# Optimization experiments

Hardware: AMD Instinct MI355X
Metric: run time of the kernel (lower is better)

The kernel has to match this reference:

```python
import jax, jax.numpy as jnp
import numpy as np

B, L, E, H, V, DT, C = 64, 80, 256, 256, 30000, 100, 4
D = 4 * L * H  # BatchNorm / FC feature dim = max_length * hidden * 4
EPS = 1e-5


def setup_inputs() -> dict:
    key = jax.random.key(0)
    ks = jax.random.split(key, 20)
    n = lambda k, shape, s: jax.random.normal(k, shape, jnp.float32) * s
    g = 1.0 / np.sqrt(H)  # pytorch LSTM init scale
    return {
        "arg1": jax.random.randint(ks[0], (B, L), 0, V, dtype=jnp.int32),
        "arg2": jax.random.randint(ks[1], (B, L), 0, V, dtype=jnp.int32),
        "seq_lengths": jnp.full((B,), L, dtype=jnp.int32),
        "transE1": jax.random.normal(ks[2], (L, DT), jnp.float32),
        "transE2": jax.random.normal(ks[3], (L, DT), jnp.float32),
        # learned parameters
        "table": n(ks[4], (V, E), 0.05),                 # embedding (xavier-ish)
        "Wih_f": n(ks[5], (4 * H, E), g),
        "Whh_f": n(ks[6], (4 * H, H), g),
        "bih_f": n(ks[7], (4 * H,), g),
        "bhh_f": n(ks[8], (4 * H,), g),
        "Wih_b": n(ks[9], (4 * H, E), g),
        "Whh_b": n(ks[10], (4 * H, H), g),
        "bih_b": n(ks[11], (4 * H,), g),
        "bhh_b": n(ks[12], (4 * H,), g),
        "R": jax.random.uniform(ks[13], (2 * E, 2 * E), jnp.float32),  # torch.rand init
        "gamma": jnp.ones((D,), jnp.float32),
        "beta": jnp.zeros((D,), jnp.float32),
        "fcW": n(ks[14], (C, D), 0.01),
        "fcb": jnp.zeros((C,), jnp.float32),
    }


def _lstm_dir(x, Wih, Whh, b):
    # x: (B, L, E); pytorch gate order i, f, g, o
    xg = jnp.einsum('ble,ge->blg', x, Wih) + b          # (B, L, 4H)
    xg = jnp.swapaxes(xg, 0, 1)                         # (L, B, 4H)
    h0 = jnp.zeros((x.shape[0], Whh.shape[1]), x.dtype)

    def step(carry, g_t):
        h, c = carry
        gates = g_t + h @ Whh.T
        i, f, gg, o = jnp.split(gates, 4, axis=-1)
        c = jax.nn.sigmoid(f) * c + jax.nn.sigmoid(i) * jnp.tanh(gg)
        h = jax.nn.sigmoid(o) * jnp.tanh(c)
        return (h, c), h

    _, hs = jax.lax.scan(step, (h0, h0), xg)
    return jnp.swapaxes(hs, 0, 1)                       # (B, L, H)


def _bilstm(x, Wih_f, Whh_f, bih_f, bhh_f, Wih_b, Whh_b, bih_b, bhh_b):
    fwd = _lstm_dir(x, Wih_f, Whh_f, bih_f + bhh_f)
    bwd = _lstm_dir(x[:, ::-1], Wih_b, Whh_b, bih_b + bhh_b)[:, ::-1]
    return jnp.concatenate([fwd, bwd], axis=-1)         # (B, L, 2H)


def _forward(arg1, arg2, transE1, transE2, table, Wih_f, Whh_f, bih_f, bhh_f,
             Wih_b, Whh_b, bih_b, bhh_b, R, gamma, beta, fcW, fcb):
    # deal_transE: relation[i,j] = tanh(mean(arg1_word_i - arg2_word_j));
    # identical for every batch element -> block-diagonal kron.
    m1 = transE1.mean(axis=1)                           # (L,)
    m2 = transE2.mean(axis=1)                           # (L,)
    rel = jnp.tanh(m1[:, None] - m2[None, :])           # (L, L)
    kg = jax.lax.stop_gradient(jnp.kron(jnp.eye(B, dtype=rel.dtype), rel))  # (B*L, B*L)

    e1 = table[arg1]                                    # (B, L, E); dropout p=0 -> identity
    e2 = table[arg2]
    o1 = _bilstm(e1, Wih_f, Whh_f, bih_f, bhh_f, Wih_b, Whh_b, bih_b, bhh_b)
    o2 = _bilstm(e2, Wih_f, Whh_f, bih_f, bhh_f, Wih_b, Whh_b, bih_b, bhh_b)

    N = B * L
    t1 = o1.reshape(N, 2 * H)
    t2 = o2.reshape(N, 2 * H)

    last = jnp.tanh((t1 @ R) @ t2.T) + kg               # (N, N)
    sf1 = jax.nn.softmax(last, axis=1).mean(axis=0)[:, None]  # (N, 1)
    sf2 = jax.nn.softmax(last, axis=0).mean(axis=1)[:, None]  # (N, 1)

    out1 = (t1 * sf2).reshape(B, L, 2 * H)
    out2 = (t2 * sf1).reshape(B, L, 2 * H)
    out = jnp.concatenate([out1, out2], axis=1).reshape(B, -1)  # (B, D)

    # BatchNorm1d in training mode (biased variance over batch)
    mu = out.mean(axis=0)
    var = out.var(axis=0)
    xn = (out - mu) / jnp.sqrt(var + EPS) * gamma + beta

    logits = xn @ fcW.T + fcb
    return jax.nn.log_softmax(logits, axis=1)           # (B, C)


def reference(arg1, arg2, seq_lengths, transE1, transE2, table, Wih_f, Whh_f,
              bih_f, bhh_f, Wih_b, Whh_b, bih_b, bhh_b, R, gamma, beta, fcW, fcb):
    del seq_lengths  # only encodes (B, L), which are static here
    return _forward(arg1, arg2, transE1, transE2, table, Wih_f, Whh_f, bih_f,
                    bhh_f, Wih_b, Whh_b, bih_b, bhh_b, R, gamma, beta, fcW, fcb)
```

## Files before the change

### kernel.cpp

```cpp
#include <hip/hip_runtime.h>
#include <cstddef>
#include <cstdint>

typedef unsigned short ushort_t;

constexpr int B_ = 64, L_ = 80, E_ = 256, H_ = 256, C_ = 4, DT_ = 100;
constexpr int N_ = B_ * L_;
constexpr int G4_ = 4 * H_;
constexpr int DH2_ = 2 * H_;
constexpr int DF_ = 4 * L_ * H_;
constexpr float EPS_ = 1e-5f;
constexpr int FB_USH = 8192;

typedef short s8v __attribute__((ext_vector_type(8)));
typedef float f4v __attribute__((ext_vector_type(4)));
typedef ushort_t us8 __attribute__((ext_vector_type(8)));

__device__ inline ushort_t f2bf_rn(float x) {
    uint32_t u = __builtin_bit_cast(uint32_t, x);
    uint32_t r = (u + 0x7fffu + ((u >> 16) & 1u)) >> 16;
    return (ushort_t)r;
}
__device__ inline float bf2f(ushort_t h) {
    uint32_t u = ((uint32_t)h) << 16;
    return __builtin_bit_cast(float, u);
}
__device__ inline float bf2f_lo(uint32_t u) { return __builtin_bit_cast(float, u << 16); }
__device__ inline float bf2f_hi(uint32_t u) { return __builtin_bit_cast(float, u & 0xffff0000u); }
__device__ inline float rcpf(float x) { return __builtin_amdgcn_rcpf(x); }
__device__ inline float sigm(float x) { return rcpf(1.f + __expf(-x)); }
__device__ inline float tanh_fast(float x) {
    float e2 = __expf(2.f * x);
    return 1.f - 2.f * rcpf(1.f + e2);
}

#define MFMA_B16(a, b, c) __builtin_amdgcn_mfma_f32_16x16x32_bf16((a), (b), (c), 0, 0, 0)

__global__ void k_prep(const int* __restrict__ arg1, const int* __restrict__ arg2,
                       const float* __restrict__ table,
                       const float* __restrict__ tE1, const float* __restrict__ tE2,
                       const float* __restrict__ Wih_f, const float* __restrict__ Wih_b,
                       const float* __restrict__ bih_f, const float* __restrict__ bhh_f,
                       const float* __restrict__ bih_b, const float* __restrict__ bhh_b,
                       const float* __restrict__ R,
                       const float* __restrict__ Whh_f, const float* __restrict__ Whh_b,
                       ushort_t* __restrict__ ehi, ushort_t* __restrict__ elo,
                       ushort_t* __restrict__ Wchi, ushort_t* __restrict__ Wclo,
                       float* __restrict__ bcat,
                       ushort_t* __restrict__ Rthi, ushort_t* __restrict__ Rtlo,
                       ushort_t* __restrict__ Bhi, ushort_t* __restrict__ Blo,
                       ushort_t* __restrict__ fragbuf, int* __restrict__ flags,
                       float* __restrict__ rel) {
    __shared__ float m1[80], m2[80];
    int blk = blockIdx.x;
    int tid = threadIdx.x;
    if (blk < 10240) {
        int r = blk;
        int rr = (r >= N_) ? (r - N_) : r;
        int idx = (r >= N_) ? arg2[rr] : arg1[rr];
        float v = table[(size_t)idx * E_ + tid];
        ushort_t h = f2bf_rn(v);
        ehi[(size_t)r * E_ + tid] = h;
        elo[(size_t)r * E_ + tid] = f2bf_rn(v - bf2f(h));
    } else if (blk < 12288) {
        int i = (blk - 10240) * 256 + tid;
        if (i < 2 * G4_ * E_) {
            float v = (i < G4_ * E_) ? Wih_f[i] : Wih_b[i - G4_ * E_];
            ushort_t h = f2bf_rn(v);
            Wchi[i] = h;
            Wclo[i] = f2bf_rn(v - bf2f(h));
        }
        if (i < 2 * G4_)
            bcat[i] = (i < G4_) ? (bih_f[i] + bhh_f[i]) : (bih_b[i - G4_] + bhh_b[i - G4_]);
        if (i < 512 * 512) {
            int m = i >> 9, k = i & 511;
            float v = R[k * 512 + m];
            ushort_t h = f2bf_rn(v);
            Rthi[i] = h;
            Rtlo[i] = f2bf_rn(v - bf2f(h));
        }
    } else if (blk < 14336) {
        int idx = (blk - 12288) * 256 + tid;
        int e = idx & 7;
        int lane = (idx >> 3) & 63;
        int g = (idx >> 9) & 3;
        int kt = (idx >> 11) & 7;
        int w = (idx >> 14) & 15;
        int d = idx >> 18;
        int c = lane & 15, q = lane >> 4;
        int row = g * 256 + w * 16 + c;
        int k = kt * 32 + q * 8 + e;
        const float* W = d ? Whh_b : Whh_f;
        float v = W[row * 256 + k];
        ushort_t hi = f2bf_rn(v);
        Bhi[idx] = hi;
        Blo[idx] = f2bf_rn(v - bf2f(hi));
    } else if (blk < 14400) {
        int i = (blk - 14336) * 256 + tid;
        if (i < 1024) flags[i] = 0;
        uint4* p = (uint4*)fragbuf;
        for (int jj = i; jj < 32768; jj += 64 * 256)
            p[jj] = make_uint4(0u, 0u, 0u, 0u);
    } else {
        if (tid < 80) {
            float s = 0.f;
            for (int k = 0; k < DT_; ++k) s += tE1[tid * DT_ + k];
            m1[tid] = s * (1.0f / DT_);
        } else if (tid < 160) {
            int i = tid - 80;
            float s = 0.f;
            for (int k = 0; k < DT_; ++k) s += tE2[i * DT_ + k];
            m2[i] = s * (1.0f / DT_);
        }
        __syncthreads();
        for (int idx = tid; idx < 80 * 80; idx += 256)
            rel[idx] = tanhf(m1[idx / 80] - m2[idx % 80]);
    }
}

__global__ __launch_bounds__(256, 2) void k_lstm9c(
        const float* __restrict__ xg,
        const ushort_t* __restrict__ Bhi, const ushort_t* __restrict__ Blo,
        ushort_t* __restrict__ o1hi, ushort_t* __restrict__ o1lo,
        ushort_t* __restrict__ o2hi, ushort_t* __restrict__ o2lo,
        ushort_t* __restrict__ fragbuf, int* __restrict__ flags) {
    const int bid = blockIdx.x;
    const int s = bid & 15;
    const int cg = (bid >> 4) & 7;
    const int d = bid >> 7;
    const int tid = threadIdx.x;
    const int g = tid >> 6, lane = tid & 63;
    const int c16 = lane & 15, qq = lane >> 4;

    __shared__ __align__(16) ushort_t Abuf[8192];
    __shared__ float pre[4][16][16];

    s8v bh[8], bl[8];
    {
        const s8v* BH = (const s8v*)Bhi;
        const s8v* BL = (const s8v*)Blo;
        int base = (d * 16 + s) * 2048 + g * 64 + lane;
        #pragma unroll
        for (int kt = 0; kt < 8; ++kt) {
            bh[kt] = BH[base + kt * 256];
            bl[kt] = BL[base + kt * 256];
        }
    }

    const int c_loc = tid >> 4, j = tid & 15;
    const int kglob = s * 16 + j;
    const int p_kt = kglob >> 5;
    const int p_q = (kglob & 31) >> 3, p_e = kglob & 7;
    const int p_lane = c_loc | (p_q << 4);
    const int fb_off = (p_kt * 64 + p_lane) * 8 + p_e;
    const int cc = cg * 16 + c_loc;
    const int w = cc >> 6, bb = cc & 63;
    ushort_t* ophi = w ? o2hi : o1hi;
    ushort_t* oplo = w ? o2lo : o1lo;
    float cst = 0.f;

    const int grp = bid >> 4;
    int* gflags = flags + grp * 16;
    const size_t fbbase = (size_t)grp * 2 * FB_USH;

    for (int t = 0; t < L_; ++t) {
        int l = d ? (L_ - 1 - t) : t;

        float xv[4];
        {
            const float* xp = xg + (size_t)(w * N_ + bb * L_ + l) * 2048
                              + d * 1024 + kglob;
            #pragma unroll
            for (int gg = 0; gg < 4; ++gg) xv[gg] = xp[gg * 256];
        }

        if (t > 0) {
            if (tid < 16) {
                while (__hip_atomic_load(&gflags[tid], __ATOMIC_RELAXED,
                                         __HIP_MEMORY_SCOPE_AGENT) < t)
                    __builtin_amdgcn_s_sleep(2);
            }
            __syncthreads();
        }

        {
            const unsigned long long* src = (const unsigned long long*)(fragbuf
                + fbbase + (size_t)(t & 1) * FB_USH);
            unsigned long long* dst = (unsigned long long*)Abuf;
            #pragma unroll
            for (int r = 0; r < 8; ++r)
                dst[r * 256 + tid] = __hip_atomic_load(
                    &src[r * 256 + tid], __ATOMIC_RELAXED,
                    __HIP_MEMORY_SCOPE_AGENT);
        }
        __syncthreads();

        f4v acc = {0.f, 0.f, 0.f, 0.f};
        {
            const s8v* AH = (const s8v*)&Abuf[0];
            const s8v* AL = (const s8v*)&Abuf[4096];
            #pragma unroll
            for (int kt = 0; kt < 8; ++kt) {
                s8v ah = AH[kt * 64 + lane];
                s8v al = AL[kt * 64 + lane];
                acc = MFMA_B16(ah, bh[kt], acc);
                acc = MFMA_B16(ah, bl[kt], acc);
                acc = MFMA_B16(al, bh[kt], acc);
            }
        }
        #pragma unroll
        for (int r = 0; r < 4; ++r)
            pre[g][qq * 4 + r][c16] = acc[r];
        __syncthreads();

        ushort_t hh, hl;
        size_t oidx;
        {
            float pi = pre[0][c_loc][j] + xv[0];
            float pf = pre[1][c_loc][j] + xv[1];
            float pg = pre[2][c_loc][j] + xv[2];
            float po = pre[3][c_loc][j] + xv[3];
            float si = sigm(pi), sf_ = sigm(pf), so = sigm(po);
            cst = sf_ * cst + si * tanh_fast(pg);
            float h = so * tanh_fast(cst);
            oidx = (size_t)(bb * L_ + l) * DH2_ + d * H_ + kglob;
            hh = f2bf_rn(h);
            hl = f2bf_rn(h - bf2f(hh));
            ushort_t* fbn = fragbuf + fbbase + (size_t)((t + 1) & 1) * FB_USH;
            __hip_atomic_store(&fbn[fb_off], hh, __ATOMIC_RELAXED,
                               __HIP_MEMORY_SCOPE_AGENT);
            __hip_atomic_store(&fbn[4096 + fb_off], hl, __ATOMIC_RELAXED,
                               __HIP_MEMORY_SCOPE_AGENT);
        }
        __syncthreads();

        if (tid == 0)
            __hip_atomic_store(&flags[bid], t + 1, __ATOMIC_RELAXED,
                               __HIP_MEMORY_SCOPE_AGENT);

        ophi[oidx] = hh;
        oplo[oidx] = hl;
    }
}

__global__ __launch_bounds__(256) void k_gemm_bf(
        const ushort_t* __restrict__ Ahi, const ushort_t* __restrict__ Alo,
        const ushort_t* __restrict__ Bthi, const ushort_t* __restrict__ Btlo,
        const float* __restrict__ bias, float* __restrict__ Cout,
        ushort_t* __restrict__ Couthi, ushort_t* __restrict__ Coutlo,
        int M, int Nn, int K) {
    __shared__ ushort_t smpool[4][4096];
    const int tid = threadIdx.x;
    const int w = tid >> 6, lane = tid & 63;
    const int wr = w >> 1, wc = w & 1;
    const int c16 = lane & 15, q4 = lane >> 4;
    const int nbx = Nn >> 7;
    const int cpx = ((M >> 7) * nbx) >> 3;
    const int fid = blockIdx.x;
    const int swz = (fid & 7) * cpx + (fid >> 3);
    const int bx = swz % nbx, by = swz / nbx;
    const int r0 = by * 128, c0 = bx * 128;

    f4v acc[4][4] = {};
    const ushort_t* planes[4] = {
        Ahi + (size_t)r0 * K, Alo + (size_t)r0 * K,
        Bthi + (size_t)c0 * K, Btlo + (size_t)c0 * K };

    for (int kk = 0; kk < K; kk += 32) {
        #pragma unroll
        for (int p = 0; p < 4; ++p) {
            const ushort_t* src = planes[p] + kk;
            #pragma unroll
            for (int it = 0; it < 2; ++it) {
                int idx = it * 256 + tid;
                int row = idx >> 2, q = idx & 3;
                *(us8*)&smpool[p][(q * 128 + row) * 8] =
                    *(const us8*)&src[(size_t)row * K + q * 8];
            }
        }
        __syncthreads();
        s8v ah[4], al[4], bhv[4], blv[4];
        #pragma unroll
        for (int mi = 0; mi < 4; ++mi) {
            int ar = wr * 64 + mi * 16 + c16;
            ah[mi] = *(const s8v*)&smpool[0][(q4 * 128 + ar) * 8];
            al[mi] = *(const s8v*)&smpool[1][(q4 * 128 + ar) * 8];
        }
        #pragma unroll
        for (int ni = 0; ni < 4; ++ni) {
            int br = wc * 64 + ni * 16 + c16;
            bhv[ni] = *(const s8v*)&smpool[2][(q4 * 128 + br) * 8];
            blv[ni] = *(const s8v*)&smpool[3][(q4 * 128 + br) * 8];
        }
        #pragma unroll
        for (int mi = 0; mi < 4; ++mi)
            #pragma unroll
            for (int ni = 0; ni < 4; ++ni) {
                acc[mi][ni] = MFMA_B16(ah[mi], bhv[ni], acc[mi][ni]);
                acc[mi][ni] = MFMA_B16(ah[mi], blv[ni], acc[mi][ni]);
                acc[mi][ni] = MFMA_B16(al[mi], bhv[ni], acc[mi][ni]);
            }
        __syncthreads();
    }
    #pragma unroll
    for (int mi = 0; mi < 4; ++mi)
        #pragma unroll
        for (int rg = 0; rg < 4; ++rg) {
            int row = r0 + wr * 64 + mi * 16 + q4 * 4 + rg;
            #pragma unroll
            for (int ni = 0; ni < 4; ++ni) {
                int col = c0 + wc * 64 + ni * 16 + c16;
                float v = acc[mi][ni][rg] + (bias ? bias[col] : 0.f);
                size_t idx = (size_t)row * Nn + col;
                if (Couthi) {
                    ushort_t h = f2bf_rn(v);
                    Couthi[idx] = h;
                    Coutlo[idx] = f2bf_rn(v - bf2f(h));
                } else {
                    Cout[idx] = v;
                }
            }
        }
}

__global__ __launch_bounds__(256) void k_bigm(
        const ushort_t* __restrict__ uhi, const ushort_t* __restrict__ ulo,
        const ushort_t* __restrict__ vhi, const ushort_t* __restrict__ vlo,
        const float* __restrict__ rel, ushort_t* __restrict__ Ebf,
        float* __restrict__ rowpart, float* __restrict__ colpart) {
    __shared__ ushort_t smpool[4][4096];
    const int tid = threadIdx.x;
    const int w = tid >> 6, lane = tid & 63;
    const int wr = w >> 1, wc = w & 1;
    const int c16 = lane & 15, q4 = lane >> 4;
    const int fid = blockIdx.x;
    const int swz = (fid & 7) * 200 + (fid >> 3);
    const int bx = swz % 40, by = swz / 40;
    const int r0 = by * 128, c0 = bx * 128;

    f4v acc[4][4] = {};
    const ushort_t* planes[4] = {
        uhi + (size_t)r0 * DH2_, ulo + (size_t)r0 * DH2_,
        vhi + (size_t)c0 * DH2_, vlo + (size_t)c0 * DH2_ };

    for (int kk = 0; kk < 16; ++kk) {
        #pragma unroll
        for (int p = 0; p < 4; ++p) {
            const ushort_t* src = planes[p] + kk * 32;
            #pragma unroll
            for (int it = 0; it < 2; ++it) {
                int idx = it * 256 + tid;
                int row = idx >> 2, q = idx & 3;
                *(us8*)&smpool[p][(q * 128 + row) * 8] =
                    *(const us8*)&src[(size_t)row * DH2_ + q * 8];
            }
        }
        __syncthreads();
        s8v ah[4], al[4], bhv[4], blv[4];
        #pragma unroll
        for (int mi = 0; mi < 4; ++mi) {
            int ar = wr * 64 + mi * 16 + c16;
            ah[mi] = *(const s8v*)&smpool[0][(q4 * 128 + ar) * 8];
            al[mi] = *(const s8v*)&smpool[1][(q4 * 128 + ar) * 8];
        }
        #pragma unroll
        for (int ni = 0; ni < 4; ++ni) {
            int br = wc * 64 + ni * 16 + c16;
            bhv[ni] = *(const s8v*)&smpool[2][(q4 * 128 + br) * 8];
            blv[ni] = *(const s8v*)&smpool[3][(q4 * 128 + br) * 8];
        }
        #pragma unroll
        for (int mi = 0; mi < 4; ++mi)
            #pragma unroll
            for (int ni = 0; ni < 4; ++ni) {
                acc[mi][ni] = MFMA_B16(ah[mi], bhv[ni], acc[mi][ni]);
                acc[mi][ni] = MFMA_B16(ah[mi], blv[ni], acc[mi][ni]);
                acc[mi][ni] = MFMA_B16(al[mi], bhv[ni], acc[mi][ni]);
            }
        __syncthreads();
    }

    float* rowred = (float*)&smpool[0][0];
    float* colred = rowred + 128 * 32;

    int gcolv[4], bjv[4], ljv[4];
    #pragma unroll
    for (int ni = 0; ni < 4; ++ni) {
        int coll = wc * 64 + ni * 16 + c16;
        gcolv[ni] = c0 + coll;
        bjv[ni] = gcolv[ni] / 80;
        ljv[ni] = gcolv[ni] - bjv[ni] * 80;
    }
    float csumv[4] = {0.f, 0.f, 0.f, 0.f};
    #pragma unroll
    for (int mi = 0; mi < 4; ++mi) {
        #pragma unroll
        for (int rg = 0; rg < 4; ++rg) {
            int rowl = wr * 64 + mi * 16 + q4 * 4 + rg;
            int grow = r0 + rowl;
            int bi = grow / 80, li = grow - bi * 80;
            float rsum = 0.f;
            #pragma unroll
            for (int ni = 0; ni < 4; ++ni) {
                float v = tanhf(acc[mi][ni][rg]);
                if (bi == bjv[ni]) v += rel[li * 80 + ljv[ni]];
                ushort_t eb = f2bf_rn(__expf(v));
                Ebf[(size_t)grow * N_ + gcolv[ni]] = eb;
                float er = bf2f(eb);
                rsum += er;
                csumv[ni] += er;
            }
            rowred[rowl * 32 + wc * 16 + c16] = rsum;
        }
    }
    #pragma unroll
    for (int ni = 0; ni < 4; ++ni) {
        int coll = wc * 64 + ni * 16 + c16;
        colred[coll * 8 + wr * 4 + q4] = csumv[ni];
    }
    __syncthreads();
    if (tid < 128) {
        float ssum = 0.f;
        #pragma unroll
        for (int t = 0; t < 32; ++t) ssum += rowred[tid * 32 + t];
        rowpart[(size_t)bx * N_ + r0 + tid] = ssum;
    } else {
        int c = tid - 128;
        float ssum = 0.f;
        #pragma unroll
        for (int t = 0; t < 8; ++t) ssum += colred[c * 8 + t];
        colpart[(size_t)by * N_ + c0 + c] = ssum;
    }
}

__global__ void k_redsum(const float* __restrict__ rowpart, const float* __restrict__ colpart,
                         float* __restrict__ rowinv, float* __restrict__ colinv) {
    int i = blockIdx.x * blockDim.x + threadIdx.x;
    if (i < N_) {
        float rs = 0.f, cs = 0.f;
        for (int t = 0; t < 40; ++t) {
            rs += rowpart[(size_t)t * N_ + i];
            cs += colpart[(size_t)t * N_ + i];
        }
        rowinv[i] = 1.f / rs;
        colinv[i] = 1.f / cs;
    }
}

__global__ __launch_bounds__(256) void k_sfboth(
        const ushort_t* __restrict__ Ebf,
        const float* __restrict__ rowinv, const float* __restrict__ colinv,
        float* __restrict__ sf1part, float* __restrict__ sf2) {
    if (blockIdx.x < N_) {
        int i = blockIdx.x;
        const uint32_t* Erow = (const uint32_t*)(Ebf + (size_t)i * N_);
        float p = 0.f;
        #pragma unroll 2
        for (int j2 = threadIdx.x; j2 < N_ / 2; j2 += 256) {
            uint32_t u = Erow[j2];
            p += bf2f_lo(u) * colinv[j2 * 2] + bf2f_hi(u) * colinv[j2 * 2 + 1];
        }
        __shared__ float red[256];
        red[threadIdx.x] = p;
        __syncthreads();
        for (int ss = 128; ss > 0; ss >>= 1) {
            if (threadIdx.x < ss) red[threadIdx.x] += red[threadIdx.x + ss];
            __syncthreads();
        }
        if (threadIdx.x == 0) sf2[i] = red[0] * (1.f / N_);
    } else {
        int b2 = blockIdx.x - N_;
        int cpb = b2 % 10, rc = b2 / 10;
        int cp = cpb * 256 + threadIdx.x;
        int r0 = rc * 320;
        float a0 = 0.f, a1 = 0.f;
        #pragma unroll 4
        for (int ii = 0; ii < 320; ++ii) {
            int row = r0 + ii;
            uint32_t u = *(const uint32_t*)(Ebf + (size_t)row * N_ + cp * 2);
            float rinv = rowinv[row];
            a0 += bf2f_lo(u) * rinv;
            a1 += bf2f_hi(u) * rinv;
        }
        sf1part[(size_t)rc * N_ + cp * 2] = a0;
        sf1part[(size_t)rc * N_ + cp * 2 + 1] = a1;
    }
}

__global__ void k_sf1red(const float* __restrict__ sf1part, float* __restrict__ sf1) {
    int jj = blockIdx.x * blockDim.x + threadIdx.x;
    if (jj < N_) {
        float s = 0.f;
        for (int t = 0; t < 16; ++t) s += sf1part[(size_t)t * N_ + jj];
        sf1[jj] = s * (1.f / N_);
    }
}

__global__ void k_bnstats(const ushort_t* __restrict__ o1hi, const ushort_t* __restrict__ o1lo,
                          const ushort_t* __restrict__ o2hi, const ushort_t* __restrict__ o2lo,
                          const float* __restrict__ sf1, const float* __restrict__ sf2,
                          float* __restrict__ bnmu, float* __restrict__ bnrstd) {
    int f = blockIdx.x * 256 + threadIdx.x;
    int seg = f / (L_ * DH2_);
    int rem = f - seg * (L_ * DH2_);
    int l = rem >> 9, hh = rem & 511;
    const ushort_t* phi = seg ? o2hi : o1hi;
    const ushort_t* plo = seg ? o2lo : o1lo;
    const float* sf = seg ? sf1 : sf2;
    float s = 0.f, s2 = 0.f;
    for (int b = 0; b < B_; ++b) {
        int row = b * L_ + l;
        size_t idx = (size_t)row * DH2_ + hh;
        float x = (bf2f(phi[idx]) + bf2f(plo[idx])) * sf[row];
        s += x;
        s2 += x * x;
    }
    float mu = s * (1.f / B_);
    float v = fmaxf(s2 * (1.f / B_) - mu * mu, 0.f);
    bnmu[f] = mu;
    bnrstd[f] = rsqrtf(v + EPS_);
}

__global__ __launch_bounds__(256) void k_logits1(
        const ushort_t* __restrict__ o1hi, const ushort_t* __restrict__ o1lo,
        const ushort_t* __restrict__ o2hi, const ushort_t* __restrict__ o2lo,
        const float* __restrict__ sf1, const float* __restrict__ sf2,
        const float* __restrict__ bnmu, const float* __restrict__ bnrstd,
        const float* __restrict__ gamma, const float* __restrict__ beta,
        const float* __restrict__ fcW, float* __restrict__ part) {
    int b = blockIdx.x, ch = blockIdx.y;
    int tid = threadIdx.x;
    int f0 = ch * (DF_ / 5);
    float acc[4] = {0.f, 0.f, 0.f, 0.f};
    for (int f = f0 + tid; f < f0 + DF_ / 5; f += 256) {
        int seg = f / (L_ * DH2_);
        int rem = f - seg * (L_ * DH2_);
        int l = rem >> 9, hh = rem & 511;
        int row = b * L_ + l;
        size_t idx = (size_t)row * DH2_ + hh;
        const ushort_t* phi = seg ? o2hi : o1hi;
        const ushort_t* plo = seg ? o2lo : o1lo;
        float val = (bf2f(phi[idx]) + bf2f(plo[idx])) * (seg ? sf1 : sf2)[row];
        float xn = (val - bnmu[f]) * bnrstd[f] * gamma[f] + beta[f];
        #pragma unroll
        for (int c = 0; c < 4; ++c) acc[c] += xn * fcW[(size_t)c * DF_ + f];
    }
    __shared__ float red[4][257];
    #pragma unroll
    for (int c = 0; c < 4; ++c) red[c][tid] = acc[c];
    __syncthreads();
    for (int ss = 128; ss > 0; ss >>= 1) {
        if (tid < ss)
            #pragma unroll
            for (int c = 0; c < 4; ++c) red[c][tid] += red[c][tid + ss];
        __syncthreads();
    }
    if (tid < 4) part[((size_t)b * 5 + ch) * 4 + tid] = red[tid][0];
}

__global__ void k_logits2(const float* __restrict__ part,
                          const float* __restrict__ fcb,
                          float* __restrict__ dout) {
    int b = blockIdx.x;
    if (threadIdx.x == 0) {
        float lg[4], mx = -1e30f;
        #pragma unroll
        for (int c = 0; c < 4; ++c) {
            float v = fcb[c];
            for (int ch = 0; ch < 5; ++ch) v += part[((size_t)b * 5 + ch) * 4 + c];
            lg[c] = v;
            mx = fmaxf(mx, v);
        }
        float se = 0.f;
        #pragma unroll
        for (int c = 0; c < 4; ++c) se += expf(lg[c] - mx);
        float lse = mx + logf(se);
        #pragma unroll
        for (int c = 0; c < 4; ++c) dout[b * 4 + c] = lg[c] - lse;
    }
}

extern "C" void kernel_launch(void* const* d_in, const int* in_sizes, int n_in,
                              void* d_out, int out_size, void* d_ws, size_t ws_size,
                              hipStream_t stream) {
    const int* arg1 = (const int*)d_in[0];
    const int* arg2 = (const int*)d_in[1];
    const float* tE1 = (const float*)d_in[3];
    const float* tE2 = (const float*)d_in[4];
    const float* table = (const float*)d_in[5];
    const float* Wih_f = (const float*)d_in[6];
    const float* Whh_f = (const float*)d_in[7];
    const float* bih_f = (const float*)d_in[8];
    const float* bhh_f = (const float*)d_in[9];
    const float* Wih_b = (const float*)d_in[10];
    const float* Whh_b = (const float*)d_in[11];
    const float* bih_b = (const float*)d_in[12];
    const float* bhh_b = (const float*)d_in[13];
    const float* R = (const float*)d_in[14];
    const float* gamma = (const float*)d_in[15];
    const float* beta = (const float*)d_in[16];
    const float* fcW = (const float*)d_in[17];
    const float* fcb = (const float*)d_in[18];
    float* dout = (float*)d_out;

    float* ws = (float*)d_ws;
    size_t off = 0;
    auto alloc = [&](size_t n) { float* p = ws + off; off += n; return p; };

    constexpr size_t PL = (size_t)N_ * DH2_;

    float* rel = alloc(80 * 80);
    float* eplanes = alloc((size_t)2 * N_ * E_);
    float* Wcplanes = alloc((size_t)2 * G4_ * E_);
    float* bcat = alloc(2 * G4_);
    float* Rtplanes = alloc((size_t)262144);
    float* planesA = alloc(PL);
    float* planesU = alloc(PL);
    float* rowpart = alloc((size_t)40 * N_);
    float* colpart = alloc((size_t)40 * N_);
    float* rowinv = alloc(N_);
    float* colinv = alloc(N_);
    float* sf1part = alloc((size_t)16 * N_);
    float* sf1 = alloc(N_);
    float* sf2 = alloc(N_);
    float* bnmu = alloc(DF_);
    float* bnrstd = alloc(DF_);
    float* lgpart = alloc((size_t)B_ * 5 * 4);
    ushort_t* Bhi = (ushort_t*)alloc(262144);
    ushort_t* Blo = (ushort_t*)alloc(262144);
    ushort_t* fragbuf = (ushort_t*)alloc(131072);
    int* flags = (int*)alloc(1024);
    float* xg = alloc((size_t)N_ * N_);
    ushort_t* Ebf = (ushort_t*)xg;

    ushort_t* ehi = (ushort_t*)eplanes;
    ushort_t* elo = ehi + (size_t)2 * N_ * E_;
    ushort_t* Wchi = (ushort_t*)Wcplanes;
    ushort_t* Wclo = Wchi + (size_t)2 * G4_ * E_;
    ushort_t* Rthi = (ushort_t*)Rtplanes;
    ushort_t* Rtlo = Rthi + 512 * 512;
    ushort_t* o1hi = (ushort_t*)planesA;
    ushort_t* o1lo = o1hi + PL;
    ushort_t* uhi = (ushort_t*)planesU;
    ushort_t* ulo = uhi + PL;
    ushort_t* o2hi = ehi;
    ushort_t* o2lo = elo;

    k_prep<<<14401, 256, 0, stream>>>(arg1, arg2, table, tE1, tE2,
                                      Wih_f, Wih_b, bih_f, bhh_f, bih_b, bhh_b,
                                      R, Whh_f, Whh_b,
                                      ehi, elo, Wchi, Wclo, bcat, Rthi, Rtlo,
                                      Bhi, Blo, fragbuf, flags, rel);
    k_gemm_bf<<<1280, 256, 0, stream>>>(
        ehi, elo, Wchi, Wclo, bcat, xg, nullptr, nullptr, 2 * N_, 2048, E_);
    k_lstm9c<<<256, 256, 0, stream>>>(xg, Bhi, Blo,
                                      o1hi, o1lo, o2hi, o2lo, fragbuf, flags);
    k_gemm_bf<<<160, 256, 0, stream>>>(
        o1hi, o1lo, Rthi, Rtlo, nullptr, nullptr, uhi, ulo, N_, 512, 512);
    k_bigm<<<1600, 256, 0, stream>>>(
        uhi, ulo, o2hi, o2lo, rel, Ebf, rowpart, colpart);
    k_redsum<<<(N_ + 255) / 256, 256, 0, stream>>>(rowpart, colpart, rowinv, colinv);
    k_sfboth<<<N_ + 160, 256, 0, stream>>>(Ebf, rowinv, colinv, sf1part, sf2);
    k_sf1red<<<(N_ + 255) / 256, 256, 0, stream>>>(sf1part, sf1);
    k_bnstats<<<DF_ / 256, 256, 0, stream>>>(o1hi, o1lo, o2hi, o2lo, sf1, sf2,
                                             bnmu, bnrstd);
    k_logits1<<<dim3(B_, 5), 256, 0, stream>>>(o1hi, o1lo, o2hi, o2lo, sf1, sf2,
                                               bnmu, bnrstd, gamma, beta, fcW, lgpart);
    k_logits2<<<B_, 64, 0, stream>>>(lgpart, fcb, dout);
}
```

Baseline: 620.7 us.

## Fuse LSTM input projection into recurrent kernel, dropping the xg GEMM

Removes the separate input-projection GEMM, which wrote a large fp32 xg buffer of gate pre-activations. The recurrent kernel now keeps the Wih fragments (hi/lo bf16 split) in registers and computes x·Wih with extra MFMAs each timestep, reading embeddings directly. This trades a full GEMM pass and the large xg write/read for more per-step compute and register pressure inside the latency-bound sequential loop. The o2 planes are also moved to their own buffer, because the embedding planes must stay live during the LSTM.

```diff
diff --git a/kernel.cpp b/kernel.cpp
--- a/kernel.cpp
+++ b/kernel.cpp
@@ -45,10 +45,10 @@
                        const float* __restrict__ R,
                        const float* __restrict__ Whh_f, const float* __restrict__ Whh_b,
                        ushort_t* __restrict__ ehi, ushort_t* __restrict__ elo,
-                       ushort_t* __restrict__ Wchi, ushort_t* __restrict__ Wclo,
                        float* __restrict__ bcat,
                        ushort_t* __restrict__ Rthi, ushort_t* __restrict__ Rtlo,
                        ushort_t* __restrict__ Bhi, ushort_t* __restrict__ Blo,
+                       ushort_t* __restrict__ Fhi, ushort_t* __restrict__ Flo,
                        ushort_t* __restrict__ fragbuf, int* __restrict__ flags,
                        float* __restrict__ rel) {
     __shared__ float m1[80], m2[80];
@@ -62,14 +62,8 @@
         ushort_t h = f2bf_rn(v);
         ehi[(size_t)r * E_ + tid] = h;
         elo[(size_t)r * E_ + tid] = f2bf_rn(v - bf2f(h));
-    } else if (blk < 12288) {
+    } else if (blk < 11264) {
         int i = (blk - 10240) * 256 + tid;
-        if (i < 2 * G4_ * E_) {
-            float v = (i < G4_ * E_) ? Wih_f[i] : Wih_b[i - G4_ * E_];
-            ushort_t h = f2bf_rn(v);
-            Wchi[i] = h;
-            Wclo[i] = f2bf_rn(v - bf2f(h));
-        }
         if (i < 2 * G4_)
             bcat[i] = (i < G4_) ? (bih_f[i] + bhh_f[i]) : (bih_b[i - G4_] + bhh_b[i - G4_]);
         if (i < 512 * 512) {
@@ -79,8 +73,8 @@
             Rthi[i] = h;
             Rtlo[i] = f2bf_rn(v - bf2f(h));
         }
-    } else if (blk < 14336) {
-        int idx = (blk - 12288) * 256 + tid;
+    } else if (blk < 13312) {
+        int idx = (blk - 11264) * 256 + tid;
         int e = idx & 7;
         int lane = (idx >> 3) & 63;
         int g = (idx >> 9) & 3;
@@ -95,8 +89,24 @@
         ushort_t hi = f2bf_rn(v);
         Bhi[idx] = hi;
         Blo[idx] = f2bf_rn(v - bf2f(hi));
-    } else if (blk < 14400) {
-        int i = (blk - 14336) * 256 + tid;
+    } else if (blk < 15360) {
+        int idx = (blk - 13312) * 256 + tid;
+        int e = idx & 7;
+        int lane = (idx >> 3) & 63;
+        int g = (idx >> 9) & 3;
+        int kt = (idx >> 11) & 7;
+        int w = (idx >> 14) & 15;
+        int d = idx >> 18;
+        int c = lane & 15, q = lane >> 4;
+        int row = g * 256 + w * 16 + c;
+        int k = kt * 32 + q * 8 + e;
+        const float* W = d ? Wih_b : Wih_f;
+        float v = W[row * 256 + k];
+        ushort_t hi = f2bf_rn(v);
+        Fhi[idx] = hi;
+        Flo[idx] = f2bf_rn(v - bf2f(hi));
+    } else if (blk < 15424) {
+        int i = (blk - 15360) * 256 + tid;
         if (i < 1024) flags[i] = 0;
         uint4* p = (uint4*)fragbuf;
         for (int jj = i; jj < 32768; jj += 64 * 256)
@@ -118,9 +128,11 @@
     }
 }
 
-__global__ __launch_bounds__(256, 2) void k_lstm9c(
-        const float* __restrict__ xg,
+__global__ __launch_bounds__(256, 2) void k_lstm10(
+        const ushort_t* __restrict__ ehi, const ushort_t* __restrict__ elo,
         const ushort_t* __restrict__ Bhi, const ushort_t* __restrict__ Blo,
+        const ushort_t* __restrict__ Fhi, const ushort_t* __restrict__ Flo,
+        const float* __restrict__ bcat,
         ushort_t* __restrict__ o1hi, ushort_t* __restrict__ o1lo,
         ushort_t* __restrict__ o2hi, ushort_t* __restrict__ o2lo,
         ushort_t* __restrict__ fragbuf, int* __restrict__ flags) {
@@ -135,15 +147,19 @@
     __shared__ __align__(16) ushort_t Abuf[8192];
     __shared__ float pre[4][16][16];
 
-    s8v bh[8], bl[8];
+    s8v bh[8], bl[8], fh[8], fl[8];
     {
         const s8v* BH = (const s8v*)Bhi;
         const s8v* BL = (const s8v*)Blo;
+        const s8v* FH = (const s8v*)Fhi;
+        const s8v* FL = (const s8v*)Flo;
         int base = (d * 16 + s) * 2048 + g * 64 + lane;
         #pragma unroll
         for (int kt = 0; kt < 8; ++kt) {
             bh[kt] = BH[base + kt * 256];
             bl[kt] = BL[base + kt * 256];
+            fh[kt] = FH[base + kt * 256];
+            fl[kt] = FL[base + kt * 256];
         }
     }
 
@@ -159,6 +175,14 @@
     ushort_t* oplo = w ? o2lo : o1lo;
     float cst = 0.f;
 
+    float bias4[4];
+    #pragma unroll
+    for (int gg = 0; gg < 4; ++gg) bias4[gg] = bcat[d * G4_ + gg * 256 + kglob];
+
+    const int ccA = cg * 16 + c16;
+    const int wA = ccA >> 6, bbA = ccA & 63;
+    const size_t erowbase = (size_t)(wA * N_ + bbA * L_) * E_ + qq * 8;
+
     const int grp = bid >> 4;
     int* gflags = flags + grp * 16;
     const size_t fbbase = (size_t)grp * 2 * FB_USH;
@@ -166,12 +190,14 @@
     for (int t = 0; t < L_; ++t) {
         int l = d ? (L_ - 1 - t) : t;
 
-        float xv[4];
+        s8v eah[8], eal[8];
         {
-            const float* xp = xg + (size_t)(w * N_ + bb * L_ + l) * 2048
-                              + d * 1024 + kglob;
-            #pragma unroll
-            for (int gg = 0; gg < 4; ++gg) xv[gg] = xp[gg * 256];
+            const size_t eoff = erowbase + (size_t)l * E_;
+            #pragma unroll
+            for (int kt = 0; kt < 8; ++kt) {
+                eah[kt] = *(const s8v*)(ehi + eoff + kt * 32);
+                eal[kt] = *(const s8v*)(elo + eoff + kt * 32);
+            }
         }
 
         if (t > 0) {
@@ -196,6 +222,12 @@
         __syncthreads();
 
         f4v acc = {0.f, 0.f, 0.f, 0.f};
+        #pragma unroll
+        for (int kt = 0; kt < 8; ++kt) {
+            acc = MFMA_B16(eah[kt], fh[kt], acc);
+            acc = MFMA_B16(eah[kt], fl[kt], acc);
+            acc = MFMA_B16(eal[kt], fh[kt], acc);
+        }
         {
             const s8v* AH = (const s8v*)&Abuf[0];
             const s8v* AL = (const s8v*)&Abuf[4096];
@@ -216,10 +248,10 @@
         ushort_t hh, hl;
         size_t oidx;
         {
-            float pi = pre[0][c_loc][j] + xv[0];
-            float pf = pre[1][c_loc][j] + xv[1];
-            float pg = pre[2][c_loc][j] + xv[2];
-            float po = pre[3][c_loc][j] + xv[3];
+            float pi = pre[0][c_loc][j] + bias4[0];
+            float pf = pre[1][c_loc][j] + bias4[1];
+            float pg = pre[2][c_loc][j] + bias4[2];
+            float po = pre[3][c_loc][j] + bias4[3];
             float si = sigm(pi), sf_ = sigm(pf), so = sigm(po);
             cst = sf_ * cst + si * tanh_fast(pg);
             float h = so * tanh_fast(cst);
@@ -611,10 +643,10 @@
 
     float* rel = alloc(80 * 80);
     float* eplanes = alloc((size_t)2 * N_ * E_);
-    float* Wcplanes = alloc((size_t)2 * G4_ * E_);
     float* bcat = alloc(2 * G4_);
     float* Rtplanes = alloc((size_t)262144);
     float* planesA = alloc(PL);
+    float* planesO2 = alloc(PL);
     float* planesU = alloc(PL);
     float* rowpart = alloc((size_t)40 * N_);
     float* colpart = alloc((size_t)40 * N_);
@@ -628,32 +660,29 @@
     float* lgpart = alloc((size_t)B_ * 5 * 4);
     ushort_t* Bhi = (ushort_t*)alloc(262144);
     ushort_t* Blo = (ushort_t*)alloc(262144);
+    ushort_t* Fhi = (ushort_t*)alloc(262144);
+    ushort_t* Flo = (ushort_t*)alloc(262144);
     ushort_t* fragbuf = (ushort_t*)alloc(131072);
     int* flags = (int*)alloc(1024);
-    float* xg = alloc((size_t)N_ * N_);
-    ushort_t* Ebf = (ushort_t*)xg;
+    ushort_t* Ebf = (ushort_t*)alloc((size_t)N_ * N_ / 2);
 
     ushort_t* ehi = (ushort_t*)eplanes;
     ushort_t* elo = ehi + (size_t)2 * N_ * E_;
-    ushort_t* Wchi = (ushort_t*)Wcplanes;
-    ushort_t* Wclo = Wchi + (size_t)2 * G4_ * E_;
     ushort_t* Rthi = (ushort_t*)Rtplanes;
     ushort_t* Rtlo = Rthi + 512 * 512;
     ushort_t* o1hi = (ushort_t*)planesA;
     ushort_t* o1lo = o1hi + PL;
+    ushort_t* o2hi = (ushort_t*)planesO2;
+    ushort_t* o2lo = o2hi + PL;
     ushort_t* uhi = (ushort_t*)planesU;
     ushort_t* ulo = uhi + PL;
-    ushort_t* o2hi = ehi;
-    ushort_t* o2lo = elo;
-
-    k_prep<<<14401, 256, 0, stream>>>(arg1, arg2, table, tE1, tE2,
+
+    k_prep<<<15425, 256, 0, stream>>>(arg1, arg2, table, tE1, tE2,
                                       Wih_f, Wih_b, bih_f, bhh_f, bih_b, bhh_b,
                                       R, Whh_f, Whh_b,
-                                      ehi, elo, Wchi, Wclo, bcat, Rthi, Rtlo,
-                                      Bhi, Blo, fragbuf, flags, rel);
-    k_gemm_bf<<<1280, 256, 0, stream>>>(
-        ehi, elo, Wchi, Wclo, bcat, xg, nullptr, nullptr, 2 * N_, 2048, E_);
-    k_lstm9c<<<256, 256, 0, stream>>>(xg, Bhi, Blo,
+                                      ehi, elo, bcat, Rthi, Rtlo,
+                                      Bhi, Blo, Fhi, Flo, fragbuf, flags, rel);
+    k_lstm10<<<256, 256, 0, stream>>>(ehi, elo, Bhi, Blo, Fhi, Flo, bcat,
                                       o1hi, o1lo, o2hi, o2lo, fragbuf, flags);
     k_gemm_bf<<<160, 256, 0, stream>>>(
         o1hi, o1lo, Rthi, Rtlo, nullptr, nullptr, uhi, ulo, N_, 512, 512);
```

Result: slower. 669.2 us (+7.8%).
